# Kernel tuning notes

Hardware: AMD Instinct MI355X
Metric: run time of the kernel (lower is better)

Reference implementation:

```python
import jax, jax.numpy as jnp
import numpy as np

B, C, H, W, N = 4, 128, 240, 320, 1024
LEVEL = 8.0          # scaling[0] = 4 * img_scale with img_scale=2
E1_LAMDA = 1.0
E2_LAMDA = 2.0 / 7.0
GN_LAMDA = 0.3
EPS = 1e-9


def extract_features(f, coords):
    # f: (B,C,H,W); coords: (B,N,2) float pixel coords as (x, y)
    Bf, Cf, Hf, Wf = f.shape
    x = coords[..., 0]
    y = coords[..., 1]
    x0 = jnp.floor(x)
    y0 = jnp.floor(y)
    wx = (x - x0)[:, None, :]          # (B,1,N)
    wy = (y - y0)[:, None, :]
    x0i = jnp.clip(x0.astype(jnp.int32), 0, Wf - 1)
    x1i = jnp.clip(x0i + 1, 0, Wf - 1)
    y0i = jnp.clip(y0.astype(jnp.int32), 0, Hf - 1)
    y1i = jnp.clip(y0i + 1, 0, Hf - 1)

    def g(fm, yi, xi):                 # fm: (C,H,W), yi/xi: (N,)
        return fm[:, yi, xi]           # (C,N)

    v00 = jax.vmap(g)(f, y0i, x0i)
    v01 = jax.vmap(g)(f, y0i, x1i)
    v10 = jax.vmap(g)(f, y1i, x0i)
    v11 = jax.vmap(g)(f, y1i, x1i)
    out = (v00 * (1 - wx) * (1 - wy) + v01 * wx * (1 - wy)
           + v10 * (1 - wx) * wy + v11 * wx * wy)          # (B,C,N)
    return out.transpose(0, 2, 1).reshape(Bf * coords.shape[1], Cf)


def l2_normalize(f):
    n = jnp.linalg.norm(f, axis=1, keepdims=True)
    return f / jnp.maximum(n, 1e-12)


def torch_gradient(f):
    # central differences with edge replication; gx = d/dx (width), gy = d/dy (height)
    fpx = jnp.pad(f, ((0, 0), (0, 0), (0, 0), (1, 1)), mode='edge')
    fpy = jnp.pad(f, ((0, 0), (0, 0), (1, 1), (0, 0)), mode='edge')
    gx = 0.5 * (fpx[..., 2:] - fpx[..., :-2])
    gy = 0.5 * (fpy[..., 2:, :] - fpy[..., :-2, :])
    return gx, gy


def compute_gn_loss(f_t, fb, ub, noise):
    Bn, Nn, _ = ub.shape
    xs = (2.0 * noise - 1.0) + ub                   # uniform(-1,1) jitter
    f_s = extract_features(fb, xs)
    f_t = l2_normalize(f_t)
    f_s = l2_normalize(f_s)
    r = f_s - f_t                                   # (BN, C)
    gx, gy = torch_gradient(fb)
    Jx = extract_features(gx, xs)                   # (BN, C)
    Jy = extract_features(gy, xs)
    J = jnp.stack([Jx, Jy], axis=-1)                # (BN, C, 2)
    Hm = jnp.einsum('bci,bcj->bij', J, J) + EPS * jnp.eye(2, dtype=J.dtype)
    b = jnp.einsum('bci,bc->bi', J, r)[..., None]   # (BN, 2, 1)
    # closed-form 2x2 inverse
    a = Hm[:, 0, 0]; bb = Hm[:, 0, 1]; c = Hm[:, 1, 0]; d = Hm[:, 1, 1]
    det = a * d - bb * c
    Hinv = jnp.stack([jnp.stack([d, -bb], -1),
                      jnp.stack([-c, a], -1)], -2) / det[:, None, None]
    miu = xs.reshape(Bn * Nn, 2, 1) - Hinv @ b
    diff = (ub.reshape(Bn * Nn, 2, 1) - miu)[..., 0]          # (BN, 2)
    e1 = 0.5 * jnp.sum(jnp.einsum('bi,bij,bj->b', diff, Hm, diff))
    log_det = jnp.log(det)
    e2 = Bn * Nn * jnp.log(jnp.asarray(2.0 * np.pi, dtype=det.dtype)) - 0.5 * jnp.sum(log_det)
    e = E1_LAMDA * e1 + E2_LAMDA * e2
    return e, e1, e2


def setup_inputs() -> dict:
    key = jax.random.key(0)
    k = jax.random.split(key, 7)
    F_a = jax.random.normal(k[0], (B, C, H, W), dtype=jnp.float32)
    F_b = jax.random.normal(k[1], (B, C, H, W), dtype=jnp.float32)
    # full-resolution match coords, safely inside the map after /LEVEL
    xa = jax.random.uniform(k[2], (B, N)) * (W - 5) * LEVEL + 2 * LEVEL
    ya = jax.random.uniform(k[3], (B, N)) * (H - 5) * LEVEL + 2 * LEVEL
    xb = jax.random.uniform(k[4], (B, N)) * (W - 5) * LEVEL + 2 * LEVEL
    yb = jax.random.uniform(k[5], (B, N)) * (H - 5) * LEVEL + 2 * LEVEL
    matches_a = jnp.stack([xa, ya], axis=-1)
    matches_b = jnp.stack([xb, yb], axis=-1)
    noise = jax.random.uniform(k[6], (B, N, 2), dtype=jnp.float32)
    return {"F_a": F_a, "F_b": F_b, "matches_a": matches_a,
            "matches_b": matches_b, "noise": noise}


def reference(F_a, F_b, matches_a, matches_b, noise):
    f_t = extract_features(F_a, matches_a / LEVEL)
    e, e1, e2 = compute_gn_loss(f_t, F_b, matches_b / LEVEL, noise)
    return GN_LAMDA * e, e1, e2
```

## Files before the change

### kernel.cpp

```cpp
#include <hip/hip_runtime.h>
#include <math.h>

#define B_  4
#define C_  128
#define H_  240
#define W_  320
#define N_  1024
#define NPTS (B_ * N_)
#define HW_ (H_ * W_)
#define NBINS 960
#define SLAB  30
#define NSLAB 8
#define LROWS 33
#define LDSF  (LROWS * W_)
#define NF4   (LDSF / 4)
#define NFB   (B_ * C_ * NSLAB)
#define NTOT  (NFB + 1024)

typedef float f4 __attribute__((ext_vector_type(4)));
typedef float f2 __attribute__((ext_vector_type(2)));

__device__ __forceinline__ f4 load4(const float* p) {
    f4 v; __builtin_memcpy(&v, p, 16); return v;
}
__device__ __forceinline__ f2 load2(const float* p) {
    f2 v; __builtin_memcpy(&v, p, 8); return v;
}

__global__ __launch_bounds__(1024) void gn_sort_kernel(
    const float* __restrict__ ma, const float* __restrict__ mb,
    const float* __restrict__ noise,
    int* __restrict__ permA, int* __restrict__ permB,
    int* __restrict__ invB, int* __restrict__ binStart)
{
    __shared__ int hist[NBINS];
    __shared__ int cursor[NBINS];

    for (int i = threadIdx.x; i < NBINS; i += 1024) hist[i] = 0;
    __syncthreads();
    int keyB[4];
    #pragma unroll
    for (int k = 0; k < 4; ++k) {
        const int p = threadIdx.x + (k << 10);
        const float ys = 2.0f * noise[p * 2 + 1] - 1.0f + mb[p * 2 + 1] * 0.125f;
        const int y0 = min(max((int)floorf(ys), 1), H_ - 3);
        keyB[k] = (p >> 10) * H_ + y0;
        atomicAdd(&hist[keyB[k]], 1);
    }
    __syncthreads();
    if (threadIdx.x < 64) {
        const int lane = threadIdx.x;
        const int base = lane * 15;
        int loc[15]; int s = 0;
        #pragma unroll
        for (int i = 0; i < 15; ++i) { loc[i] = s; s += hist[base + i]; }
        int incl = s;
        #pragma unroll
        for (int off = 1; off < 64; off <<= 1) {
            const int v = __shfl_up(incl, off, 64);
            if (lane >= off) incl += v;
        }
        const int excl = incl - s;
        #pragma unroll
        for (int i = 0; i < 15; ++i) cursor[base + i] = excl + loc[i];
    }
    __syncthreads();
    for (int i = threadIdx.x; i < NBINS; i += 1024) binStart[i] = cursor[i];
    if (threadIdx.x == 0) binStart[NBINS] = NPTS;
    __syncthreads();
    #pragma unroll
    for (int k = 0; k < 4; ++k) {
        const int p = threadIdx.x + (k << 10);
        const int pos = atomicAdd(&cursor[keyB[k]], 1);
        permB[pos] = p;
        invB[p] = pos;
    }
    __syncthreads();

    for (int i = threadIdx.x; i < NBINS; i += 1024) hist[i] = 0;
    __syncthreads();
    int keyA[4];
    #pragma unroll
    for (int k = 0; k < 4; ++k) {
        const int p = threadIdx.x + (k << 10);
        const float ya = ma[p * 2 + 1] * 0.125f;
        const int y0 = min(max((int)floorf(ya), 0), H_ - 2);
        keyA[k] = (p >> 10) * H_ + y0;
        atomicAdd(&hist[keyA[k]], 1);
    }
    __syncthreads();
    if (threadIdx.x < 64) {
        const int lane = threadIdx.x;
        const int base = lane * 15;
        int loc[15]; int s = 0;
        #pragma unroll
        for (int i = 0; i < 15; ++i) { loc[i] = s; s += hist[base + i]; }
        int incl = s;
        #pragma unroll
        for (int off = 1; off < 64; off <<= 1) {
            const int v = __shfl_up(incl, off, 64);
            if (lane >= off) incl += v;
        }
        const int excl = incl - s;
        #pragma unroll
        for (int i = 0; i < 15; ++i) cursor[base + i] = excl + loc[i];
    }
    __syncthreads();
    #pragma unroll
    for (int k = 0; k < 4; ++k) {
        const int p = threadIdx.x + (k << 10);
        permA[atomicAdd(&cursor[keyA[k]], 1)] = p;
    }
}

__global__ __launch_bounds__(256) void gn_gather_kernel(
    const float* __restrict__ Fa, const float* __restrict__ Fb,
    const float* __restrict__ ma, const float* __restrict__ mb,
    const float* __restrict__ noise,
    const int* __restrict__ permA, const int* __restrict__ permB,
    const int* __restrict__ invB, const int* __restrict__ binStart,
    float* __restrict__ ws_ft, float* __restrict__ fjp)
{
    __shared__ float rows[LDSF];
    const int tid = threadIdx.x;
    const int bid = blockIdx.x;

    if ((bid % 5) != 4) {
        const int blk = bid - bid / 5;
        const int c  = blk & (C_ - 1);
        const int bs = blk >> 7;
        const int b  = bs >> 3;
        const int s  = bs & (NSLAB - 1);
        const int ybase = s * SLAB - 1;

        const float* __restrict__ plane = Fb + ((size_t)(b * C_ + c)) * HW_;
        const int srcbase = ybase * W_;

        f4 tmp[11];
        #pragma unroll
        for (int k = 0; k < 11; ++k) {
            const int slot = tid + (k << 8);
            int src = srcbase + (slot << 2);
            src = min(max(src, 0), HW_ - 4);
            tmp[k] = load4(plane + src);
        }
        #pragma unroll
        for (int k = 0; k < 11; ++k) {
            const int slot = tid + (k << 8);
            if (slot < NF4) *(f4*)&rows[slot << 2] = tmp[k];
        }
        __syncthreads();

        const int binbase = b * H_ + s * SLAB;
        const int pLo = binStart[binbase];
        const int pHi = binStart[binbase + SLAB];

        for (int i = pLo + tid; i < pHi; i += 256) {
            const int p = permB[i];
            const float ubx = mb[p * 2 + 0] * 0.125f;
            const float uby = mb[p * 2 + 1] * 0.125f;
            const float xs  = 2.0f * noise[p * 2 + 0] - 1.0f + ubx;
            const float ys  = 2.0f * noise[p * 2 + 1] - 1.0f + uby;

            const float bx0f = floorf(xs), by0f = floorf(ys);
            const float wx = xs - bx0f, wy = ys - by0f;
            const int x0 = min(max((int)bx0f, 1), W_ - 3);
            const int y0 = min(max((int)by0f, 1), H_ - 3);
            const int rel = y0 - ybase;

            const float* rY0 = &rows[rel * W_];
            const float* rY1 = rY0 + W_;
            const float* rYm = rY0 - W_;
            const float* rYp = rY1 + W_;

            const float r0m = rY0[x0 - 1], r00 = rY0[x0];
            const float r01 = rY0[x0 + 1], r0p = rY0[x0 + 2];
            const float r1m = rY1[x0 - 1], r10 = rY1[x0];
            const float r11 = rY1[x0 + 1], r1p = rY1[x0 + 2];
            const float rm0 = rYm[x0],     rm1 = rYm[x0 + 1];
            const float rp0 = rYp[x0],     rp1 = rYp[x0 + 1];

            const float w00 = (1.f - wx) * (1.f - wy);
            const float w01 = wx * (1.f - wy);
            const float w10 = (1.f - wx) * wy;
            const float w11 = wx * wy;

            const float fs = r00 * w00 + r01 * w01 + r10 * w10 + r11 * w11;
            const float jx = 0.5f * ((r01 - r0m) * w00 + (r0p - r00) * w01
                                   + (r11 - r1m) * w10 + (r1p - r10) * w11);
            const float jy = 0.5f * ((r10 - rm0) * w00 + (r11 - rm1) * w01
                                   + (rp0 - r00) * w10 + (rp1 - r01) * w11);

            const size_t base = (size_t)c * 3 * NPTS + i;
            fjp[base]            = fs;
            fjp[base + NPTS]     = jx;
            fjp[base + 2 * NPTS] = jy;
        }
    } else {
        const int fi   = bid / 5;
        const int w    = (fi << 2) | (tid >> 6);
        const int lane = tid & 63;
        const int pg   = w >> 6;
        const int c0   = (w & 63) << 1;
        const int p    = permA[(pg << 6) | lane];
        const int b    = p >> 10;

        const float xa = ma[p * 2 + 0] * 0.125f;
        const float ya = ma[p * 2 + 1] * 0.125f;
        const float ax0f = floorf(xa), ay0f = floorf(ya);
        const float awx = xa - ax0f, awy = ya - ay0f;
        const int ax0 = min(max((int)ax0f, 0), W_ - 2);
        const int ay0 = min(max((int)ay0f, 0), H_ - 2);
        const int o0 = ay0 * W_ + ax0;
        const int o1 = o0 + W_;

        const float* __restrict__ fa0 = Fa + ((size_t)(b * C_ + c0)) * HW_;
        const float* __restrict__ fa1 = fa0 + HW_;

        const f2 a0_0 = load2(fa0 + o0);
        const f2 a1_0 = load2(fa0 + o1);
        const f2 a0_1 = load2(fa1 + o0);
        const f2 a1_1 = load2(fa1 + o1);

        const float w00 = (1.f - awx) * (1.f - awy);
        const float w01 = awx * (1.f - awy);
        const float w10 = (1.f - awx) * awy;
        const float w11 = awx * awy;

        const float ft0 = a0_0.x * w00 + a0_0.y * w01 + a1_0.x * w10 + a1_0.y * w11;
        const float ft1 = a0_1.x * w00 + a0_1.y * w01 + a1_1.x * w10 + a1_1.y * w11;

        const int slot = invB[p];
        ws_ft[(size_t)c0 * NPTS + slot]       = ft0;
        ws_ft[(size_t)(c0 + 1) * NPTS + slot] = ft1;
    }
}

__global__ __launch_bounds__(64) void gn_combine_kernel(
    const float* __restrict__ ws_ft, const float* __restrict__ fjp,
    const float* __restrict__ mb, const float* __restrict__ noise,
    const int* __restrict__ permB,
    float* __restrict__ ws_e1, float* __restrict__ ws_ld)
{
    const int i = blockIdx.x * 64 + threadIdx.x;
    const int p = permB[i];

    float s[9];
    #pragma unroll
    for (int k = 0; k < 9; ++k) s[k] = 0.f;

    #pragma unroll 4
    for (int c = 0; c < C_; ++c) {
        const float ft = ws_ft[(size_t)c * NPTS + i];
        const size_t base = (size_t)c * 3 * NPTS + i;
        const float fs = fjp[base];
        const float jx = fjp[base + NPTS];
        const float jy = fjp[base + 2 * NPTS];
        s[0] += ft * ft;
        s[1] += fs * fs;
        s[2] += jx * fs;
        s[3] += jx * ft;
        s[4] += jy * fs;
        s[5] += jy * ft;
        s[6] += jx * jx;
        s[7] += jx * jy;
        s[8] += jy * jy;
    }

    const float ubx = mb[p * 2 + 0] * 0.125f;
    const float uby = mb[p * 2 + 1] * 0.125f;
    const float xs  = 2.0f * noise[p * 2 + 0] - 1.0f + ubx;
    const float ys  = 2.0f * noise[p * 2 + 1] - 1.0f + uby;

    const float nt = fmaxf(sqrtf(s[0]), 1e-12f);
    const float ns = fmaxf(sqrtf(s[1]), 1e-12f);
    const float b0 = s[2] / ns - s[3] / nt;
    const float b1 = s[4] / ns - s[5] / nt;
    const float H00 = s[6] + 1e-9f;
    const float H01 = s[7];
    const float H11 = s[8] + 1e-9f;
    const float det = H00 * H11 - H01 * H01;
    const float inv = 1.0f / det;
    const float u0 = (H11 * b0 - H01 * b1) * inv;
    const float u1 = (H00 * b1 - H01 * b0) * inv;
    const float d0 = (ubx - xs) + u0;
    const float d1 = (uby - ys) + u1;
    const float quad = d0 * (H00 * d0 + H01 * d1) + d1 * (H01 * d0 + H11 * d1);
    ws_e1[p] = 0.5f * quad;
    ws_ld[p] = logf(det);
}

__global__ __launch_bounds__(256) void gn_reduce_kernel(
    const float* __restrict__ ws_e1, const float* __restrict__ ws_ld,
    float* __restrict__ out)
{
    __shared__ double sm1[256];
    __shared__ double sm2[256];
    double a1 = 0.0, a2 = 0.0;
    for (int i = threadIdx.x; i < NPTS; i += 256) {
        a1 += (double)ws_e1[i];
        a2 += (double)ws_ld[i];
    }
    sm1[threadIdx.x] = a1;
    sm2[threadIdx.x] = a2;
    __syncthreads();
    for (int s = 128; s > 0; s >>= 1) {
        if (threadIdx.x < s) {
            sm1[threadIdx.x] += sm1[threadIdx.x + s];
            sm2[threadIdx.x] += sm2[threadIdx.x + s];
        }
        __syncthreads();
    }
    if (threadIdx.x == 0) {
        const double e1 = sm1[0];
        const double sum_ld = sm2[0];
        const double log2pi = (double)logf(6.283185307179586f);
        const double e2 = (double)NPTS * log2pi - 0.5 * sum_ld;
        const double e = 1.0 * e1 + (2.0 / 7.0) * e2;
        out[0] = (float)(0.3 * e);
        out[1] = (float)e1;
        out[2] = (float)e2;
    }
}

extern "C" void kernel_launch(void* const* d_in, const int* in_sizes, int n_in,
                              void* d_out, int out_size, void* d_ws, size_t ws_size,
                              hipStream_t stream) {
    const float* Fa    = (const float*)d_in[0];
    const float* Fb    = (const float*)d_in[1];
    const float* ma    = (const float*)d_in[2];
    const float* mb    = (const float*)d_in[3];
    const float* noise = (const float*)d_in[4];
    float* out = (float*)d_out;

    float* ws_e1    = (float*)d_ws;
    float* ws_ld    = ws_e1 + NPTS;
    int*   permA    = (int*)(ws_ld + NPTS);
    int*   permB    = permA + NPTS;
    int*   invB     = permB + NPTS;
    int*   binStart = invB + NPTS;
    float* ws_ft    = (float*)(binStart + 1024);
    float* fjp      = ws_ft + (size_t)C_ * NPTS;

    gn_sort_kernel<<<1, 1024, 0, stream>>>(ma, mb, noise, permA, permB,
                                           invB, binStart);
    gn_gather_kernel<<<NTOT, 256, 0, stream>>>(Fa, Fb, ma, mb, noise,
                                               permA, permB, invB,
                                               binStart, ws_ft, fjp);
    gn_combine_kernel<<<NPTS / 64, 64, 0, stream>>>(ws_ft, fjp, mb, noise,
                                                    permB, ws_e1, ws_ld);
    gn_reduce_kernel<<<1, 256, 0, stream>>>(ws_e1, ws_ld, out);
}
```

Measured before the change: 79.19 us.

## Stream F_b plane through LDS slabs with prefetch; presort coordinates in sort kernel

Each F_b block now owns a whole (batch, channel) plane and walks through 12 slabs of 20 rows, prefetching the next slab into registers while computing the current one. Before, each slab was its own block and loaded halo rows separately. The sort kernel now writes the jittered sample coordinates, target coordinates and a packed A-to-B slot map in sorted order. This removes the permutation and indirect coordinate gathers in the main and combine kernels. The cost is far fewer F_b blocks (512 instead of 4096), which lowers parallelism and occupancy, plus a serial loop with extra barriers.

New measurement: 89.88 us. 13.5% more time.

```diff
diff --git a/kernel.cpp b/kernel.cpp
--- a/kernel.cpp
+++ b/kernel.cpp
@@ -9,13 +9,12 @@
 #define NPTS (B_ * N_)
 #define HW_ (H_ * W_)
 #define NBINS 960
-#define SLAB  30
-#define NSLAB 8
-#define LROWS 33
-#define LDSF  (LROWS * W_)
-#define NF4   (LDSF / 4)
-#define NFB   (B_ * C_ * NSLAB)
-#define NTOT  (NFB + 1024)
+#define SH    20
+#define NSLB  12
+#define BROWS 23
+#define BF4   ((BROWS * W_) / 4)
+#define NFA   1024
+#define NFBK  512
 
 typedef float f4 __attribute__((ext_vector_type(4)));
 typedef float f2 __attribute__((ext_vector_type(2)));
@@ -30,21 +29,27 @@
 __global__ __launch_bounds__(1024) void gn_sort_kernel(
     const float* __restrict__ ma, const float* __restrict__ mb,
     const float* __restrict__ noise,
-    int* __restrict__ permA, int* __restrict__ permB,
-    int* __restrict__ invB, int* __restrict__ binStart)
+    int* __restrict__ permB, int* __restrict__ binStart,
+    float* __restrict__ xsys, float* __restrict__ ubuv,
+    float* __restrict__ xaya, int* __restrict__ a2b)
 {
     __shared__ int hist[NBINS];
     __shared__ int cursor[NBINS];
 
     for (int i = threadIdx.x; i < NBINS; i += 1024) hist[i] = 0;
     __syncthreads();
-    int keyB[4];
+    int keyB[4], slotB[4];
+    float vxs[4], vys[4], vux[4], vuy[4];
     #pragma unroll
     for (int k = 0; k < 4; ++k) {
         const int p = threadIdx.x + (k << 10);
-        const float ys = 2.0f * noise[p * 2 + 1] - 1.0f + mb[p * 2 + 1] * 0.125f;
+        const float ubx = mb[p * 2 + 0] * 0.125f;
+        const float uby = mb[p * 2 + 1] * 0.125f;
+        const float xs  = 2.0f * noise[p * 2 + 0] - 1.0f + ubx;
+        const float ys  = 2.0f * noise[p * 2 + 1] - 1.0f + uby;
         const int y0 = min(max((int)floorf(ys), 1), H_ - 3);
         keyB[k] = (p >> 10) * H_ + y0;
+        vxs[k] = xs; vys[k] = ys; vux[k] = ubx; vuy[k] = uby;
         atomicAdd(&hist[keyB[k]], 1);
     }
     __syncthreads();
@@ -73,19 +78,26 @@
         const int p = threadIdx.x + (k << 10);
         const int pos = atomicAdd(&cursor[keyB[k]], 1);
         permB[pos] = p;
-        invB[p] = pos;
+        xsys[2 * pos]     = vxs[k];
+        xsys[2 * pos + 1] = vys[k];
+        ubuv[2 * pos]     = vux[k];
+        ubuv[2 * pos + 1] = vuy[k];
+        slotB[k] = pos;
     }
     __syncthreads();
 
     for (int i = threadIdx.x; i < NBINS; i += 1024) hist[i] = 0;
     __syncthreads();
     int keyA[4];
+    float vxa[4], vya[4];
     #pragma unroll
     for (int k = 0; k < 4; ++k) {
         const int p = threadIdx.x + (k << 10);
+        const float xa = ma[p * 2 + 0] * 0.125f;
         const float ya = ma[p * 2 + 1] * 0.125f;
-        const int y0 = min(max((int)floorf(ya), 0), H_ - 2);
-        keyA[k] = (p >> 10) * H_ + y0;
+        const int ay0 = min(max((int)floorf(ya), 0), H_ - 2);
+        keyA[k] = (p >> 10) * H_ + ay0;
+        vxa[k] = xa; vya[k] = ya;
         atomicAdd(&hist[keyA[k]], 1);
     }
     __syncthreads();
@@ -109,104 +121,37 @@
     #pragma unroll
     for (int k = 0; k < 4; ++k) {
         const int p = threadIdx.x + (k << 10);
-        permA[atomicAdd(&cursor[keyA[k]], 1)] = p;
-    }
-}
-
-__global__ __launch_bounds__(256) void gn_gather_kernel(
+        const int pos = atomicAdd(&cursor[keyA[k]], 1);
+        xaya[2 * pos]     = vxa[k];
+        xaya[2 * pos + 1] = vya[k];
+        a2b[pos] = ((p >> 10) << 16) | slotB[k];
+    }
+}
+
+__global__ __launch_bounds__(256) void gn_main_kernel(
     const float* __restrict__ Fa, const float* __restrict__ Fb,
-    const float* __restrict__ ma, const float* __restrict__ mb,
-    const float* __restrict__ noise,
-    const int* __restrict__ permA, const int* __restrict__ permB,
-    const int* __restrict__ invB, const int* __restrict__ binStart,
+    const int* __restrict__ binStart,
+    const float* __restrict__ xsys, const float* __restrict__ xaya,
+    const int* __restrict__ a2b,
     float* __restrict__ ws_ft, float* __restrict__ fjp)
 {
-    __shared__ float rows[LDSF];
+    __shared__ float buf[BROWS * W_];
     const int tid = threadIdx.x;
     const int bid = blockIdx.x;
 
-    if ((bid % 5) != 4) {
-        const int blk = bid - bid / 5;
-        const int c  = blk & (C_ - 1);
-        const int bs = blk >> 7;
-        const int b  = bs >> 3;
-        const int s  = bs & (NSLAB - 1);
-        const int ybase = s * SLAB - 1;
-
-        const float* __restrict__ plane = Fb + ((size_t)(b * C_ + c)) * HW_;
-        const int srcbase = ybase * W_;
-
-        f4 tmp[11];
-        #pragma unroll
-        for (int k = 0; k < 11; ++k) {
-            const int slot = tid + (k << 8);
-            int src = srcbase + (slot << 2);
-            src = min(max(src, 0), HW_ - 4);
-            tmp[k] = load4(plane + src);
-        }
-        #pragma unroll
-        for (int k = 0; k < 11; ++k) {
-            const int slot = tid + (k << 8);
-            if (slot < NF4) *(f4*)&rows[slot << 2] = tmp[k];
-        }
-        __syncthreads();
-
-        const int binbase = b * H_ + s * SLAB;
-        const int pLo = binStart[binbase];
-        const int pHi = binStart[binbase + SLAB];
-
-        for (int i = pLo + tid; i < pHi; i += 256) {
-            const int p = permB[i];
-            const float ubx = mb[p * 2 + 0] * 0.125f;
-            const float uby = mb[p * 2 + 1] * 0.125f;
-            const float xs  = 2.0f * noise[p * 2 + 0] - 1.0f + ubx;
-            const float ys  = 2.0f * noise[p * 2 + 1] - 1.0f + uby;
-
-            const float bx0f = floorf(xs), by0f = floorf(ys);
-            const float wx = xs - bx0f, wy = ys - by0f;
-            const int x0 = min(max((int)bx0f, 1), W_ - 3);
-            const int y0 = min(max((int)by0f, 1), H_ - 3);
-            const int rel = y0 - ybase;
-
-            const float* rY0 = &rows[rel * W_];
-            const float* rY1 = rY0 + W_;
-            const float* rYm = rY0 - W_;
-            const float* rYp = rY1 + W_;
-
-            const float r0m = rY0[x0 - 1], r00 = rY0[x0];
-            const float r01 = rY0[x0 + 1], r0p = rY0[x0 + 2];
-            const float r1m = rY1[x0 - 1], r10 = rY1[x0];
-            const float r11 = rY1[x0 + 1], r1p = rY1[x0 + 2];
-            const float rm0 = rYm[x0],     rm1 = rYm[x0 + 1];
-            const float rp0 = rYp[x0],     rp1 = rYp[x0 + 1];
-
-            const float w00 = (1.f - wx) * (1.f - wy);
-            const float w01 = wx * (1.f - wy);
-            const float w10 = (1.f - wx) * wy;
-            const float w11 = wx * wy;
-
-            const float fs = r00 * w00 + r01 * w01 + r10 * w10 + r11 * w11;
-            const float jx = 0.5f * ((r01 - r0m) * w00 + (r0p - r00) * w01
-                                   + (r11 - r1m) * w10 + (r1p - r10) * w11);
-            const float jy = 0.5f * ((r10 - rm0) * w00 + (r11 - rm1) * w01
-                                   + (rp0 - r00) * w10 + (rp1 - r01) * w11);
-
-            const size_t base = (size_t)c * 3 * NPTS + i;
-            fjp[base]            = fs;
-            fjp[base + NPTS]     = jx;
-            fjp[base + 2 * NPTS] = jy;
-        }
-    } else {
-        const int fi   = bid / 5;
-        const int w    = (fi << 2) | (tid >> 6);
+    if (bid < NFA) {
+        const int w    = (bid << 2) | (tid >> 6);
         const int lane = tid & 63;
         const int pg   = w >> 6;
         const int c0   = (w & 63) << 1;
-        const int p    = permA[(pg << 6) | lane];
-        const int b    = p >> 10;
-
-        const float xa = ma[p * 2 + 0] * 0.125f;
-        const float ya = ma[p * 2 + 1] * 0.125f;
+        const int ai   = (pg << 6) | lane;
+
+        const f2 xy   = load2(xaya + 2 * ai);
+        const int meta = a2b[ai];
+        const int b     = meta >> 16;
+        const int slotB = meta & 0xFFFF;
+
+        const float xa = xy.x, ya = xy.y;
         const float ax0f = floorf(xa), ay0f = floorf(ya);
         const float awx = xa - ax0f, awy = ya - ay0f;
         const int ax0 = min(max((int)ax0f, 0), W_ - 2);
@@ -230,20 +175,97 @@
         const float ft0 = a0_0.x * w00 + a0_0.y * w01 + a1_0.x * w10 + a1_0.y * w11;
         const float ft1 = a0_1.x * w00 + a0_1.y * w01 + a1_1.x * w10 + a1_1.y * w11;
 
-        const int slot = invB[p];
-        ws_ft[(size_t)c0 * NPTS + slot]       = ft0;
-        ws_ft[(size_t)(c0 + 1) * NPTS + slot] = ft1;
+        ws_ft[(size_t)c0 * NPTS + slotB]       = ft0;
+        ws_ft[(size_t)(c0 + 1) * NPTS + slotB] = ft1;
+    } else {
+        const int blk = bid - NFA;
+        const int c = blk & (C_ - 1);
+        const int b = blk >> 7;
+        const float* __restrict__ plane = Fb + ((size_t)(b * C_ + c)) * HW_;
+
+        f4 tmp[8];
+        {
+            const int sbase = -W_;
+            #pragma unroll
+            for (int k = 0; k < 8; ++k) {
+                int src = sbase + ((tid + (k << 8)) << 2);
+                src = min(max(src, 0), HW_ - 4);
+                tmp[k] = load4(plane + src);
+            }
+        }
+
+        for (int t = 0; t < NSLB; ++t) {
+            #pragma unroll
+            for (int k = 0; k < 8; ++k) {
+                const int slot = tid + (k << 8);
+                if (slot < BF4) *(f4*)&buf[slot << 2] = tmp[k];
+            }
+            __syncthreads();
+
+            if (t + 1 < NSLB) {
+                const int sbase = ((t + 1) * SH - 1) * W_;
+                #pragma unroll
+                for (int k = 0; k < 8; ++k) {
+                    int src = sbase + ((tid + (k << 8)) << 2);
+                    src = min(max(src, 0), HW_ - 4);
+                    tmp[k] = load4(plane + src);
+                }
+            }
+
+            const int binbase = b * H_ + t * SH;
+            const int pLo = binStart[binbase];
+            const int pHi = binStart[binbase + SH];
+            const int ybase = t * SH - 1;
+
+            for (int i = pLo + tid; i < pHi; i += 256) {
+                const f2 sc = load2(xsys + 2 * i);
+                const float xs = sc.x, ys = sc.y;
+                const float bx0f = floorf(xs), by0f = floorf(ys);
+                const float wx = xs - bx0f, wy = ys - by0f;
+                const int x0 = min(max((int)bx0f, 1), W_ - 3);
+                const int y0 = min(max((int)by0f, 1), H_ - 3);
+                const int rel = y0 - ybase;
+
+                const float* rY0 = &buf[rel * W_];
+                const float* rY1 = rY0 + W_;
+                const float* rYm = rY0 - W_;
+                const float* rYp = rY1 + W_;
+
+                const float r0m = rY0[x0 - 1], r00 = rY0[x0];
+                const float r01 = rY0[x0 + 1], r0p = rY0[x0 + 2];
+                const float r1m = rY1[x0 - 1], r10 = rY1[x0];
+                const float r11 = rY1[x0 + 1], r1p = rY1[x0 + 2];
+                const float rm0 = rYm[x0],     rm1 = rYm[x0 + 1];
+                const float rp0 = rYp[x0],     rp1 = rYp[x0 + 1];
+
+                const float w00 = (1.f - wx) * (1.f - wy);
+                const float w01 = wx * (1.f - wy);
+                const float w10 = (1.f - wx) * wy;
+                const float w11 = wx * wy;
+
+                const float fs = r00 * w00 + r01 * w01 + r10 * w10 + r11 * w11;
+                const float jx = 0.5f * ((r01 - r0m) * w00 + (r0p - r00) * w01
+                                       + (r11 - r1m) * w10 + (r1p - r10) * w11);
+                const float jy = 0.5f * ((r10 - rm0) * w00 + (r11 - rm1) * w01
+                                       + (rp0 - r00) * w10 + (rp1 - r01) * w11);
+
+                const size_t base = (size_t)c * 3 * NPTS + i;
+                fjp[base]            = fs;
+                fjp[base + NPTS]     = jx;
+                fjp[base + 2 * NPTS] = jy;
+            }
+            __syncthreads();
+        }
     }
 }
 
 __global__ __launch_bounds__(64) void gn_combine_kernel(
     const float* __restrict__ ws_ft, const float* __restrict__ fjp,
-    const float* __restrict__ mb, const float* __restrict__ noise,
+    const float* __restrict__ xsys, const float* __restrict__ ubuv,
     const int* __restrict__ permB,
     float* __restrict__ ws_e1, float* __restrict__ ws_ld)
 {
     const int i = blockIdx.x * 64 + threadIdx.x;
-    const int p = permB[i];
 
     float s[9];
     #pragma unroll
@@ -267,10 +289,10 @@
         s[8] += jy * jy;
     }
 
-    const float ubx = mb[p * 2 + 0] * 0.125f;
-    const float uby = mb[p * 2 + 1] * 0.125f;
-    const float xs  = 2.0f * noise[p * 2 + 0] - 1.0f + ubx;
-    const float ys  = 2.0f * noise[p * 2 + 1] - 1.0f + uby;
+    const f2 uu = load2(ubuv + 2 * i);
+    const f2 sc = load2(xsys + 2 * i);
+    const float ubx = uu.x, uby = uu.y;
+    const float xs = sc.x, ys = sc.y;
 
     const float nt = fmaxf(sqrtf(s[0]), 1e-12f);
     const float ns = fmaxf(sqrtf(s[1]), 1e-12f);
@@ -286,6 +308,8 @@
     const float d0 = (ubx - xs) + u0;
     const float d1 = (uby - ys) + u1;
     const float quad = d0 * (H00 * d0 + H01 * d1) + d1 * (H01 * d0 + H11 * d1);
+
+    const int p = permB[i];
     ws_e1[p] = 0.5f * quad;
     ws_ld[p] = logf(det);
 }
@@ -335,19 +359,21 @@
 
     float* ws_e1    = (float*)d_ws;
     float* ws_ld    = ws_e1 + NPTS;
-    int*   permA    = (int*)(ws_ld + NPTS);
-    int*   permB    = permA + NPTS;
-    int*   invB     = permB + NPTS;
-    int*   binStart = invB + NPTS;
-    float* ws_ft    = (float*)(binStart + 1024);
+    int*   permB    = (int*)(ws_ld + NPTS);
+    int*   binStart = permB + NPTS;
+    int*   a2b      = binStart + 1024;
+    float* xsys     = (float*)(a2b + NPTS);
+    float* ubuv     = xsys + 2 * NPTS;
+    float* xaya     = ubuv + 2 * NPTS;
+    float* ws_ft    = xaya + 2 * NPTS;
     float* fjp      = ws_ft + (size_t)C_ * NPTS;
 
-    gn_sort_kernel<<<1, 1024, 0, stream>>>(ma, mb, noise, permA, permB,
-                                           invB, binStart);
-    gn_gather_kernel<<<NTOT, 256, 0, stream>>>(Fa, Fb, ma, mb, noise,
-                                               permA, permB, invB,
-                                               binStart, ws_ft, fjp);
-    gn_combine_kernel<<<NPTS / 64, 64, 0, stream>>>(ws_ft, fjp, mb, noise,
+    gn_sort_kernel<<<1, 1024, 0, stream>>>(ma, mb, noise, permB, binStart,
+                                           xsys, ubuv, xaya, a2b);
+    gn_main_kernel<<<NFA + NFBK, 256, 0, stream>>>(Fa, Fb, binStart,
+                                                   xsys, xaya, a2b,
+                                                   ws_ft, fjp);
+    gn_combine_kernel<<<NPTS / 64, 64, 0, stream>>>(ws_ft, fjp, xsys, ubuv,
                                                     permB, ws_e1, ws_ld);
     gn_reduce_kernel<<<1, 256, 0, stream>>>(ws_e1, ws_ld, out);
 }
```
